# Kernel tuning notes

Measured on AMD Instinct MI355X. Metric: run time of the kernel, lower is better.

## Reference

```python
import jax, jax.numpy as jnp
import numpy as np

N_HEAD = 16
D_MODEL = 1024
D_HEAD = D_MODEL // N_HEAD  # 64
B, S = 1, 4096


def setup_inputs() -> dict:
    key = jax.random.key(0)
    ks = jax.random.split(key, 7)
    q = jax.random.normal(ks[0], (B, S, D_MODEL), dtype=jnp.float32)
    k = jax.random.normal(ks[1], (B, S, D_MODEL), dtype=jnp.float32)
    v = jax.random.normal(ks[2], (B, S, D_MODEL), dtype=jnp.float32)
    mask = jnp.ones((S, S), dtype=bool)
    # params match torch.rand init (uniform [0,1)); use uniform here too
    w_q = jax.random.uniform(ks[3], (D_MODEL, D_MODEL), dtype=jnp.float32)
    w_k = jax.random.uniform(ks[4], (D_HEAD, D_MODEL), dtype=jnp.float32)
    w_v = jax.random.uniform(ks[5], (D_HEAD, D_MODEL), dtype=jnp.float32)
    w_out = jax.random.uniform(ks[6], (D_MODEL, D_MODEL), dtype=jnp.float32)
    return {"q": q, "k": k, "v": v, "mask": mask,
            "w_q": w_q, "w_k": w_k, "w_v": w_v, "w_out": w_out}


def reference(q, k, v, mask, w_q, w_k, w_v, w_out):
    # F.linear(x, W) == x @ W.T
    query = q @ w_q.T                      # [b, n, d_model]
    key = k @ w_k.T                        # [b, s, d_head]  (single shared KV head)
    value = v @ w_v.T                      # [b, s, d_head]
    b, n, _ = query.shape
    query = query.reshape(b, n, N_HEAD, D_HEAD).transpose(0, 2, 1, 3)  # b h n d
    scores = jnp.einsum('bhnd,bsd->bhns', query, key) / jnp.sqrt(jnp.float32(D_HEAD))
    scores = jnp.where(mask[None, None], scores, jnp.float32(-jnp.inf))
    attn = jax.nn.softmax(scores, axis=-1)             # [b, h, n, s]
    out = jnp.einsum('bhns,bsd->bhnd', attn, value)    # [b, h, n, d]
    out = out.transpose(0, 2, 1, 3).reshape(b, n, D_MODEL)
    return out @ w_out.T
```

## Files before the change

kernel.cpp:

```cpp
#include <hip/hip_runtime.h>
#include <cstdint>
#include <cstddef>

#define S_LEN   4096
#define DM      1024
#define NHEAD   16
#define DH      64
#define SPLITS  4

typedef short bf16x8 __attribute__((ext_vector_type(8)));
typedef _Float16 f16x8 __attribute__((ext_vector_type(8)));
typedef float f32x4  __attribute__((ext_vector_type(4)));

__device__ __forceinline__ unsigned short f2bf(float x) {
    uint32_t u = __float_as_uint(x);
    u += 0x7fffu + ((u >> 16) & 1u);
    return (unsigned short)(u >> 16);
}
__device__ __forceinline__ float bf2f(unsigned short u) {
    return __uint_as_float(((uint32_t)u) << 16);
}
__device__ __forceinline__ unsigned pack_bf2(float a, float b) {
    return (unsigned)f2bf(a) | ((unsigned)f2bf(b) << 16);
}
__device__ __forceinline__ unsigned short f2h(float x) {
    _Float16 h = (_Float16)x;
    return __builtin_bit_cast(unsigned short, h);
}
__device__ __forceinline__ unsigned pack_h2(float a, float b) {
    return __builtin_bit_cast(unsigned, __builtin_amdgcn_cvt_pkrtz(a, b));
}
__device__ __forceinline__ void gl_lds16(const unsigned short* g, unsigned short* l) {
    __builtin_amdgcn_global_load_lds(
        (const __attribute__((address_space(1))) unsigned int*)g,
        (__attribute__((address_space(3))) unsigned int*)l, 16, 0, 0);
}
__device__ __forceinline__ void split8(const float4& a0, const float4& a1,
                                       ushort4& h0, ushort4& h1,
                                       ushort4& l0, ushort4& l1) {
    h0.x = f2bf(a0.x); l0.x = f2bf(a0.x - bf2f(h0.x));
    h0.y = f2bf(a0.y); l0.y = f2bf(a0.y - bf2f(h0.y));
    h0.z = f2bf(a0.z); l0.z = f2bf(a0.z - bf2f(h0.z));
    h0.w = f2bf(a0.w); l0.w = f2bf(a0.w - bf2f(h0.w));
    h1.x = f2bf(a1.x); l1.x = f2bf(a1.x - bf2f(h1.x));
    h1.y = f2bf(a1.y); l1.y = f2bf(a1.y - bf2f(h1.y));
    h1.z = f2bf(a1.z); l1.z = f2bf(a1.z - bf2f(h1.z));
    h1.w = f2bf(a1.w); l1.w = f2bf(a1.w - bf2f(h1.w));
}

__launch_bounds__(256)
__global__ void pre_kernel(const float* __restrict__ kin, const float* __restrict__ vin,
                           const float* __restrict__ wk, const float* __restrict__ wv,
                           const float* __restrict__ q, const float* __restrict__ wq,
                           const float* __restrict__ wo,
                           unsigned short* __restrict__ Kf, unsigned short* __restrict__ Vtf,
                           unsigned short* __restrict__ qh, unsigned short* __restrict__ ql,
                           unsigned short* __restrict__ wqh, unsigned short* __restrict__ wql,
                           unsigned short* __restrict__ woh)
{
    __shared__ unsigned short As_h[64][72];
    __shared__ unsigned short Bs_h[64][72];
    __shared__ unsigned short As_l[64][72];
    __shared__ unsigned short Bs_l[64][72];

    const int tid = threadIdx.x;
    const int bx  = blockIdx.x;

    if (bx >= 128) {
        const int G1 = 1048576, GW = 262144;
        int i = (bx - 128) * 256 + tid;
        const float* src; unsigned short* h; unsigned short* l = nullptr; int off;
        if (i < G1)            { src = q;  h = qh;  l = ql;  off = i; }
        else if (i < G1 + GW)  { src = wq; h = wqh; l = wql; off = i - G1; }
        else                   { src = wo; h = woh;          off = i - G1 - GW; }
        float4 vv = reinterpret_cast<const float4*>(src)[off];
        ushort4 hh;
        hh.x = f2bf(vv.x); hh.y = f2bf(vv.y); hh.z = f2bf(vv.z); hh.w = f2bf(vv.w);
        reinterpret_cast<ushort4*>(h)[off] = hh;
        if (l) {
            ushort4 ll;
            ll.x = f2bf(vv.x - bf2f(hh.x)); ll.y = f2bf(vv.y - bf2f(hh.y));
            ll.z = f2bf(vv.z - bf2f(hh.z)); ll.w = f2bf(vv.w - bf2f(hh.w));
            reinterpret_cast<ushort4*>(l)[off] = ll;
        }
        return;
    }

    const int wave = tid >> 6;
    const int lane = tid & 63;
    const int lm   = lane & 15;
    const int quad = lane >> 4;
    const bool isK = (bx < 64);
    const int m0   = (bx & 63) * 64;
    const float* A = isK ? kin : vin;
    const float* B = isK ? wk : wv;

    f32x4 acc[4] = {};

    for (int kc = 0; kc < DM; kc += 64) {
        __syncthreads();
#pragma unroll
        for (int i = 0; i < 2; ++i) {
            int c   = tid + i * 256;
            int r   = c >> 3;
            int col = (c & 7) * 8;
            float4 a0 = *(const float4*)&A[(size_t)(m0 + r) * DM + kc + col];
            float4 a1 = *(const float4*)&A[(size_t)(m0 + r) * DM + kc + col + 4];
            float4 b0 = *(const float4*)&B[(size_t)r * DM + kc + col];
            float4 b1 = *(const float4*)&B[(size_t)r * DM + kc + col + 4];
            ushort4 h0, h1, l0, l1;
            split8(a0, a1, h0, h1, l0, l1);
            *(ushort4*)&As_h[r][col] = h0;  *(ushort4*)&As_h[r][col + 4] = h1;
            if (isK) { *(ushort4*)&As_l[r][col] = l0;  *(ushort4*)&As_l[r][col + 4] = l1; }
            split8(b0, b1, h0, h1, l0, l1);
            *(ushort4*)&Bs_h[r][col] = h0;  *(ushort4*)&Bs_h[r][col + 4] = h1;
            if (isK) { *(ushort4*)&Bs_l[r][col] = l0;  *(ushort4*)&Bs_l[r][col + 4] = l1; }
        }
        __syncthreads();
#pragma unroll
        for (int kk = 0; kk < 64; kk += 32) {
            bf16x8 bh = *(const bf16x8*)&Bs_h[wave * 16 + lm][kk + quad * 8];
            bf16x8 bl;
            if (isK) bl = *(const bf16x8*)&Bs_l[wave * 16 + lm][kk + quad * 8];
#pragma unroll
            for (int ms = 0; ms < 4; ++ms) {
                bf16x8 ah = *(const bf16x8*)&As_h[ms * 16 + lm][kk + quad * 8];
                acc[ms] = __builtin_amdgcn_mfma_f32_16x16x32_bf16(ah, bh, acc[ms], 0, 0, 0);
                if (isK) {
                    bf16x8 al = *(const bf16x8*)&As_l[ms * 16 + lm][kk + quad * 8];
                    acc[ms] = __builtin_amdgcn_mfma_f32_16x16x32_bf16(ah, bl, acc[ms], 0, 0, 0);
                    acc[ms] = __builtin_amdgcn_mfma_f32_16x16x32_bf16(al, bh, acc[ms], 0, 0, 0);
                }
            }
        }
    }

#pragma unroll
    for (int ms = 0; ms < 4; ++ms)
#pragma unroll
        for (int r = 0; r < 4; ++r) {
            int row = m0 + ms * 16 + quad * 4 + r;
            int col = wave * 16 + lm;
            if (isK) Kf[(size_t)row * DH + col] = f2h(acc[ms][r]);
            else     Vtf[(size_t)col * S_LEN + row] = f2h(acc[ms][r]);
        }
}

__launch_bounds__(256)
__global__ void gemm_big(const unsigned short* __restrict__ Ah,
                         const unsigned short* __restrict__ Al,
                         const unsigned short* __restrict__ Bh,
                         const unsigned short* __restrict__ Bl,
                         unsigned short* __restrict__ Ch,
                         int M, int N, int K, int ldc)
{
    __shared__ unsigned short As_h[2][8192];
    __shared__ unsigned short Bs_h[2][8192];
    __shared__ unsigned short As_l[2][8192];
    __shared__ unsigned short Bs_l[2][8192];

    const int tid  = threadIdx.x;
    const int wave = tid >> 6;
    const int lane = tid & 63;
    const int lm   = lane & 15;
    const int quad = lane >> 4;
    const int wm   = wave >> 1;
    const int wn   = wave & 1;
    const int m0   = blockIdx.x * 128;
    const int n0   = blockIdx.y * 128;

    int srow[4], scol[4];
#pragma unroll
    for (int i = 0; i < 4; ++i) {
        int f = i * 256 + tid;
        srow[i] = f >> 3;
        scol[i] = ((f & 7) ^ (srow[i] & 7)) * 8;
    }

    auto stage = [&](int b, int kc) {
#pragma unroll
        for (int i = 0; i < 4; ++i) {
            const int dst = (i * 256 + wave * 64) * 8;
            gl_lds16(&Ah[(size_t)(m0 + srow[i]) * K + kc + scol[i]], &As_h[b][dst]);
            gl_lds16(&Bh[(size_t)(n0 + srow[i]) * K + kc + scol[i]], &Bs_h[b][dst]);
            gl_lds16(&Al[(size_t)(m0 + srow[i]) * K + kc + scol[i]], &As_l[b][dst]);
            gl_lds16(&Bl[(size_t)(n0 + srow[i]) * K + kc + scol[i]], &Bs_l[b][dst]);
        }
    };

    stage(0, 0);

    f32x4 acc[4][4] = {};
    const int nkc = K / 64;

    for (int it = 0; it < nkc; ++it) {
        const int b = it & 1;
        __syncthreads();
        if (it + 1 < nkc) stage(b ^ 1, (it + 1) * 64);

#pragma unroll
        for (int kk = 0; kk < 2; ++kk) {
            bf16x8 bh[4], bl[4];
#pragma unroll
            for (int ns = 0; ns < 4; ++ns) {
                const int off = (wn * 64 + ns * 16 + lm) * 64 + ((kk * 4 + quad) ^ (lm & 7)) * 8;
                bh[ns] = *(const bf16x8*)&Bs_h[b][off];
                bl[ns] = *(const bf16x8*)&Bs_l[b][off];
            }
#pragma unroll
            for (int ms = 0; ms < 4; ++ms) {
                const int off = (wm * 64 + ms * 16 + lm) * 64 + ((kk * 4 + quad) ^ (lm & 7)) * 8;
                bf16x8 ah = *(const bf16x8*)&As_h[b][off];
                bf16x8 al = *(const bf16x8*)&As_l[b][off];
#pragma unroll
                for (int ns = 0; ns < 4; ++ns) {
                    acc[ms][ns] = __builtin_amdgcn_mfma_f32_16x16x32_bf16(ah, bh[ns], acc[ms][ns], 0, 0, 0);
                    acc[ms][ns] = __builtin_amdgcn_mfma_f32_16x16x32_bf16(ah, bl[ns], acc[ms][ns], 0, 0, 0);
                    acc[ms][ns] = __builtin_amdgcn_mfma_f32_16x16x32_bf16(al, bh[ns], acc[ms][ns], 0, 0, 0);
                }
            }
        }
    }

#pragma unroll
    for (int ms = 0; ms < 4; ++ms)
#pragma unroll
        for (int ns = 0; ns < 4; ++ns)
#pragma unroll
            for (int r = 0; r < 4; ++r) {
                int row = m0 + wm * 64 + ms * 16 + quad * 4 + r;
                int col = n0 + wn * 64 + ns * 16 + lm;
                Ch[(size_t)row * ldc + col] = f2h(acc[ms][ns][r]);
            }
}

__launch_bounds__(256)
__global__ void flash_kernel(const unsigned short* __restrict__ Qf,
                             const unsigned short* __restrict__ Kf,
                             const unsigned short* __restrict__ Vt,
                             unsigned short* __restrict__ Op,
                             float* __restrict__ Mb,
                             float* __restrict__ Lb)
{
    __shared__ unsigned short Ks[2][4096];
    __shared__ unsigned short Vs[2][4096];

    const int tid  = threadIdx.x;
    const int wave = tid >> 6;
    const int lane = tid & 63;
    const int lm   = lane & 15;
    const int quad = lane >> 4;
    const int q0   = blockIdx.x * 128;
    const int h    = blockIdx.y;
    const int sp   = blockIdx.z;
    const int kbase = sp * (S_LEN / SPLITS);
    const int NIT  = S_LEN / SPLITS / 64;
    const float c  = 0.125f * 1.44269504f;

    const int r0 = tid >> 3,         c0 = ((tid & 7) ^ (r0 & 7)) * 8;
    const int r1 = (tid + 256) >> 3, c1 = ((tid & 7) ^ (r1 & 7)) * 8;
    const int ldsA = wave * 512;
    const int ldsB = 2048 + wave * 512;

    auto stage = [&](int kt, int b) {
        gl_lds16(&Kf[(size_t)(kt + r0) * DH + c0], &Ks[b][ldsA]);
        gl_lds16(&Kf[(size_t)(kt + r1) * DH + c1], &Ks[b][ldsB]);
        gl_lds16(&Vt[(size_t)r0 * S_LEN + kt + c0], &Vs[b][ldsA]);
        gl_lds16(&Vt[(size_t)r1 * S_LEN + kt + c1], &Vs[b][ldsB]);
    };

    stage(kbase, 0);

    f16x8 qf[2][2];
#pragma unroll
    for (int nb = 0; nb < 2; ++nb)
#pragma unroll
        for (int kk = 0; kk < 2; ++kk) {
            size_t idx = (size_t)(q0 + wave * 32 + nb * 16 + lm) * DM + h * DH + kk * 32 + quad * 8;
            qf[nb][kk] = *(const f16x8*)&Qf[idx];
        }

    f32x4 oacc[2][4] = {};
    float m_run[2] = {-1e30f, -1e30f}, l_run[2] = {0.f, 0.f};

    for (int it = 0; it < NIT; ++it) {
        const int b = it & 1;
        const int kt = kbase + it * 64;
        __syncthreads();
        if (it + 1 < NIT) stage(kt + 64, b ^ 1);

        f32x4 sacc[2][4] = {};
#pragma unroll
        for (int kk = 0; kk < 2; ++kk) {
#pragma unroll
            for (int ms = 0; ms < 4; ++ms) {
                const int off = (ms * 16 + lm) * 64 + ((4 * kk + quad) ^ (lm & 7)) * 8;
                f16x8 kfr = *(const f16x8*)&Ks[b][off];
#pragma unroll
                for (int nb = 0; nb < 2; ++nb)
                    sacc[nb][ms] = __builtin_amdgcn_mfma_f32_16x16x32_f16(kfr, qf[nb][kk], sacc[nb][ms], 0, 0, 0);
            }
        }

        float mn[2];
#pragma unroll
        for (int nb = 0; nb < 2; ++nb) {
            float mx = -1e30f;
#pragma unroll
            for (int ms = 0; ms < 4; ++ms)
#pragma unroll
                for (int r = 0; r < 4; ++r) mx = fmaxf(mx, sacc[nb][ms][r]);
            mx = fmaxf(mx, __shfl_xor(mx, 16));
            mx = fmaxf(mx, __shfl_xor(mx, 32));
            mn[nb] = fmaxf(m_run[nb], mx);
        }

        if (__any((mn[0] > m_run[0]) || (mn[1] > m_run[1]))) {
#pragma unroll
            for (int mq = 0; mq < 2; ++mq) {
                float alpha = __builtin_amdgcn_exp2f((m_run[mq] - mn[mq]) * c);
                l_run[mq] *= alpha;
                m_run[mq] = mn[mq];
                float ar[4];
#pragma unroll
                for (int r = 0; r < 4; ++r) ar[r] = __shfl(alpha, quad * 4 + r);
#pragma unroll
                for (int nd = 0; nd < 4; ++nd)
#pragma unroll
                    for (int r = 0; r < 4; ++r) oacc[mq][nd][r] *= ar[r];
            }
        }

        unsigned pk[2][4][2];
#pragma unroll
        for (int nb = 0; nb < 2; ++nb) {
            float mc = m_run[nb] * c;
            float ps = 0.f;
#pragma unroll
            for (int ms = 0; ms < 4; ++ms) {
                float pr[4];
#pragma unroll
                for (int r = 0; r < 4; ++r) {
                    pr[r] = __builtin_amdgcn_exp2f(fmaf(sacc[nb][ms][r], c, -mc));
                    ps += pr[r];
                }
                pk[nb][ms][0] = pack_h2(pr[0], pr[1]);
                pk[nb][ms][1] = pack_h2(pr[2], pr[3]);
            }
            ps += __shfl_xor(ps, 16);
            ps += __shfl_xor(ps, 32);
            l_run[nb] += ps;
        }

#pragma unroll
        for (int kb = 0; kb < 2; ++kb) {
            f16x8 pa[2];
#pragma unroll
            for (int nb = 0; nb < 2; ++nb) {
                unsigned af[4] __attribute__((aligned(16)));
#pragma unroll
                for (int d = 0; d < 4; ++d) {
                    int srcl = ((2 * quad + (d >> 1)) & 3) * 16 + lm;
                    unsigned v_lo = (unsigned)__shfl((int)pk[nb][2 * kb][d & 1], srcl);
                    unsigned v_hi = (unsigned)__shfl((int)pk[nb][2 * kb + 1][d & 1], srcl);
                    af[d] = (quad < 2) ? v_lo : v_hi;
                }
                pa[nb] = *(f16x8*)af;
            }
#pragma unroll
            for (int nd = 0; nd < 4; ++nd) {
                const int off = (nd * 16 + lm) * 64 + ((4 * kb + quad) ^ (lm & 7)) * 8;
                f16x8 vb = *(const f16x8*)&Vs[b][off];
#pragma unroll
                for (int nb = 0; nb < 2; ++nb)
                    oacc[nb][nd] = __builtin_amdgcn_mfma_f32_16x16x32_f16(pa[nb], vb, oacc[nb][nd], 0, 0, 0);
            }
        }
    }

    unsigned short* Osp = Op + (size_t)sp * NHEAD * S_LEN * DH;
#pragma unroll
    for (int mq = 0; mq < 2; ++mq) {
#pragma unroll
        for (int nd = 0; nd < 4; ++nd)
#pragma unroll
            for (int r = 0; r < 4; ++r) {
                int q = q0 + wave * 32 + mq * 16 + quad * 4 + r;
                Osp[((size_t)h * S_LEN + q) * DH + nd * 16 + lm] = f2bf(oacc[mq][nd][r]);
            }
        if (quad == 0) {
            int q = q0 + wave * 32 + mq * 16 + lm;
            Mb[(size_t)sp * NHEAD * S_LEN + h * S_LEN + q] = m_run[mq];
            Lb[(size_t)sp * NHEAD * S_LEN + h * S_LEN + q] = l_run[mq];
        }
    }
}

__launch_bounds__(256)
__global__ void out_proj(const unsigned short* __restrict__ Op,
                         const float* __restrict__ Mb,
                         const float* __restrict__ Lb,
                         const unsigned short* __restrict__ Wo,
                         float* __restrict__ out)
{
    __shared__ unsigned short As[64][72];
    __shared__ unsigned short Bs[128][72];

    const int tid  = threadIdx.x;
    const int wave = tid >> 6;
    const int lane = tid & 63;
    const int lm   = lane & 15;
    const int quad = lane >> 4;
    const int m0   = blockIdx.x * 64;
    const int n0   = blockIdx.y * 128;
    const float c  = 0.125f * 1.44269504f;
    const int HS   = NHEAD * S_LEN;
    const size_t OSP = (size_t)NHEAD * S_LEN * DH;

    f32x4 acc[4][2] = {};

    for (int it = 0; it < 16; ++it) {
        __syncthreads();
#pragma unroll
        for (int i = 0; i < 2; ++i) {
            int cc  = tid + i * 256;
            int r   = cc >> 3;
            int col = (cc & 7) * 8;
            int q   = m0 + r;
            int hq  = it * S_LEN + q;
            float m_i[SPLITS], l_i[SPLITS];
            float mm = -1e30f;
#pragma unroll
            for (int s = 0; s < SPLITS; ++s) {
                m_i[s] = Mb[s * HS + hq];
                l_i[s] = Lb[s * HS + hq];
                mm = fmaxf(mm, m_i[s]);
            }
            float w_i[SPLITS], denom = 0.f;
#pragma unroll
            for (int s = 0; s < SPLITS; ++s) {
                w_i[s] = __builtin_amdgcn_exp2f((m_i[s] - mm) * c);
                denom += l_i[s] * w_i[s];
            }
            float inv = 1.0f / denom;
#pragma unroll
            for (int s = 0; s < SPLITS; ++s) w_i[s] *= inv;

            size_t base = ((size_t)it * S_LEN + q) * DH + col;
            uint4 u[SPLITS];
#pragma unroll
            for (int s = 0; s < SPLITS; ++s) u[s] = *(const uint4*)&Op[s * OSP + base];
            unsigned mrg[4];
#pragma unroll
            for (int d = 0; d < 4; ++d) {
                float a = 0.f, b = 0.f;
#pragma unroll
                for (int s = 0; s < SPLITS; ++s) {
                    unsigned uu = ((const unsigned*)&u[s])[d];
                    a = fmaf(bf2f((unsigned short)(uu & 0xffff)), w_i[s], a);
                    b = fmaf(bf2f((unsigned short)(uu >> 16)),    w_i[s], b);
                }
                mrg[d] = pack_bf2(a, b);
            }
            *(uint4*)&As[r][col] = *(uint4*)mrg;
        }
#pragma unroll
        for (int i = 0; i < 4; ++i) {
            int cc  = tid + i * 256;
            int r   = cc >> 3;
            int col = (cc & 7) * 8;
            *(uint4*)&Bs[r][col] = *(const uint4*)&Wo[(size_t)(n0 + r) * DM + it * 64 + col];
        }
        __syncthreads();
#pragma unroll
        for (int kk = 0; kk < 64; kk += 32) {
            bf16x8 bh[2];
#pragma unroll
            for (int ns = 0; ns < 2; ++ns)
                bh[ns] = *(const bf16x8*)&Bs[wave * 32 + ns * 16 + lm][kk + quad * 8];
#pragma unroll
            for (int ms = 0; ms < 4; ++ms) {
                bf16x8 ah = *(const bf16x8*)&As[ms * 16 + lm][kk + quad * 8];
#pragma unroll
                for (int ns = 0; ns < 2; ++ns)
                    acc[ms][ns] = __builtin_amdgcn_mfma_f32_16x16x32_bf16(ah, bh[ns], acc[ms][ns], 0, 0, 0);
            }
        }
    }

#pragma unroll
    for (int ms = 0; ms < 4; ++ms)
#pragma unroll
        for (int ns = 0; ns < 2; ++ns)
#pragma unroll
            for (int r = 0; r < 4; ++r) {
                int row = m0 + ms * 16 + quad * 4 + r;
                int col = n0 + wave * 32 + ns * 16 + lm;
                out[(size_t)row * DM + col] = acc[ms][ns][r];
            }
}

extern "C" void kernel_launch(void* const* d_in, const int* in_sizes, int n_in,
                              void* d_out, int out_size, void* d_ws, size_t ws_size,
                              hipStream_t stream)
{
    (void)in_sizes; (void)n_in; (void)out_size; (void)ws_size;
    const float* q     = (const float*)d_in[0];
    const float* k     = (const float*)d_in[1];
    const float* v     = (const float*)d_in[2];
    const float* w_q   = (const float*)d_in[4];
    const float* w_k   = (const float*)d_in[5];
    const float* w_v   = (const float*)d_in[6];
    const float* w_out = (const float*)d_in[7];
    float* out = (float*)d_out;

    char* ws = (char*)d_ws;
    size_t off = 0;
    auto alloc = [&](size_t bytes) -> unsigned short* {
        unsigned short* p = (unsigned short*)(ws + off);
        off += (bytes + 255) & ~(size_t)255;
        return p;
    };
    const size_t SZ_QKV = (size_t)S_LEN * DM * 2;
    const size_t SZ_WQ  = (size_t)DM * DM * 2;
    const size_t SZ_KV  = (size_t)S_LEN * DH * 2;

    unsigned short* qh  = alloc(SZ_QKV);
    unsigned short* ql  = alloc(SZ_QKV);
    unsigned short* wqh = alloc(SZ_WQ);
    unsigned short* wql = alloc(SZ_WQ);
    unsigned short* woh = alloc(SZ_WQ);
    unsigned short* Qf  = alloc(SZ_QKV);
    unsigned short* Kf  = alloc(SZ_KV);
    unsigned short* Vtf = alloc(SZ_KV);
    unsigned short* Op  = alloc(SPLITS * NHEAD * SZ_KV);
    float* Mb = (float*)alloc(SPLITS * NHEAD * S_LEN * 4);
    float* Lb = (float*)alloc(SPLITS * NHEAD * S_LEN * 4);

    pre_kernel<<<dim3(6272), 256, 0, stream>>>(k, v, w_k, w_v, q, w_q, w_out,
                                               Kf, Vtf, qh, ql, wqh, wql, woh);

    gemm_big<<<dim3(32, 8), 256, 0, stream>>>(qh, ql, wqh, wql, Qf, S_LEN, DM, DM, DM);

    flash_kernel<<<dim3(32, 16, SPLITS), 256, 0, stream>>>(Qf, Kf, Vtf, Op, Mb, Lb);

    out_proj<<<dim3(64, 8), 256, 0, stream>>>(Op, Mb, Lb, woh, out);
}
```

Before: 397.7 us.

## Double KV tile to 128 keys per iteration and halve split-K count

```diff
diff --git a/kernel.cpp b/kernel.cpp
--- a/kernel.cpp
+++ b/kernel.cpp
@@ -6,7 +6,7 @@
 #define DM      1024
 #define NHEAD   16
 #define DH      64
-#define SPLITS  4
+#define SPLITS  2
 
 typedef short bf16x8 __attribute__((ext_vector_type(8)));
 typedef _Float16 f16x8 __attribute__((ext_vector_type(8)));
@@ -242,8 +242,8 @@
                              float* __restrict__ Mb,
                              float* __restrict__ Lb)
 {
-    __shared__ unsigned short Ks[2][4096];
-    __shared__ unsigned short Vs[2][4096];
+    __shared__ unsigned short Ks[2][8192];
+    __shared__ unsigned short Vs[2][8192];
 
     const int tid  = threadIdx.x;
     const int wave = tid >> 6;
@@ -254,19 +254,24 @@
     const int h    = blockIdx.y;
     const int sp   = blockIdx.z;
     const int kbase = sp * (S_LEN / SPLITS);
-    const int NIT  = S_LEN / SPLITS / 64;
+    const int NIT  = S_LEN / SPLITS / 128;
     const float c  = 0.125f * 1.44269504f;
 
-    const int r0 = tid >> 3,         c0 = ((tid & 7) ^ (r0 & 7)) * 8;
-    const int r1 = (tid + 256) >> 3, c1 = ((tid & 7) ^ (r1 & 7)) * 8;
-    const int ldsA = wave * 512;
-    const int ldsB = 2048 + wave * 512;
+    int kr[4], kcol[4], vr[4], vcol[4];
+#pragma unroll
+    for (int i = 0; i < 4; ++i) {
+        int f = i * 256 + tid;
+        kr[i] = f >> 3;  kcol[i] = ((f & 7) ^ (kr[i] & 7)) * 8;
+        vr[i] = f >> 4;  vcol[i] = ((f & 15) ^ (vr[i] & 15)) * 8;
+    }
 
     auto stage = [&](int kt, int b) {
-        gl_lds16(&Kf[(size_t)(kt + r0) * DH + c0], &Ks[b][ldsA]);
-        gl_lds16(&Kf[(size_t)(kt + r1) * DH + c1], &Ks[b][ldsB]);
-        gl_lds16(&Vt[(size_t)r0 * S_LEN + kt + c0], &Vs[b][ldsA]);
-        gl_lds16(&Vt[(size_t)r1 * S_LEN + kt + c1], &Vs[b][ldsB]);
+#pragma unroll
+        for (int i = 0; i < 4; ++i) {
+            const int dst = (i * 256 + wave * 64) * 8;
+            gl_lds16(&Kf[(size_t)(kt + kr[i]) * DH + kcol[i]], &Ks[b][dst]);
+            gl_lds16(&Vt[(size_t)vr[i] * S_LEN + kt + vcol[i]], &Vs[b][dst]);
+        }
     };
 
     stage(kbase, 0);
@@ -285,31 +290,34 @@
 
     for (int it = 0; it < NIT; ++it) {
         const int b = it & 1;
-        const int kt = kbase + it * 64;
+        const int kt = kbase + it * 128;
         __syncthreads();
-        if (it + 1 < NIT) stage(kt + 64, b ^ 1);
-
-        f32x4 sacc[2][4] = {};
-#pragma unroll
-        for (int kk = 0; kk < 2; ++kk) {
-#pragma unroll
-            for (int ms = 0; ms < 4; ++ms) {
-                const int off = (ms * 16 + lm) * 64 + ((4 * kk + quad) ^ (lm & 7)) * 8;
-                f16x8 kfr = *(const f16x8*)&Ks[b][off];
-#pragma unroll
-                for (int nb = 0; nb < 2; ++nb)
-                    sacc[nb][ms] = __builtin_amdgcn_mfma_f32_16x16x32_f16(kfr, qf[nb][kk], sacc[nb][ms], 0, 0, 0);
-            }
-        }
+        if (it + 1 < NIT) stage(kt + 128, b ^ 1);
+
+        f32x4 sacc[2][2][4] = {};
+#pragma unroll
+        for (int t = 0; t < 2; ++t)
+#pragma unroll
+            for (int kk = 0; kk < 2; ++kk)
+#pragma unroll
+                for (int ms = 0; ms < 4; ++ms) {
+                    const int off = (t * 64 + ms * 16 + lm) * 64 + ((4 * kk + quad) ^ (lm & 7)) * 8;
+                    f16x8 kfr = *(const f16x8*)&Ks[b][off];
+#pragma unroll
+                    for (int nb = 0; nb < 2; ++nb)
+                        sacc[nb][t][ms] = __builtin_amdgcn_mfma_f32_16x16x32_f16(kfr, qf[nb][kk], sacc[nb][t][ms], 0, 0, 0);
+                }
 
         float mn[2];
 #pragma unroll
         for (int nb = 0; nb < 2; ++nb) {
             float mx = -1e30f;
 #pragma unroll
-            for (int ms = 0; ms < 4; ++ms)
-#pragma unroll
-                for (int r = 0; r < 4; ++r) mx = fmaxf(mx, sacc[nb][ms][r]);
+            for (int t = 0; t < 2; ++t)
+#pragma unroll
+                for (int ms = 0; ms < 4; ++ms)
+#pragma unroll
+                    for (int r = 0; r < 4; ++r) mx = fmaxf(mx, sacc[nb][t][ms][r]);
             mx = fmaxf(mx, __shfl_xor(mx, 16));
             mx = fmaxf(mx, __shfl_xor(mx, 32));
             mn[nb] = fmaxf(m_run[nb], mx);
@@ -331,51 +339,56 @@
             }
         }
 
-        unsigned pk[2][4][2];
+        unsigned pk[2][2][4][2];
 #pragma unroll
         for (int nb = 0; nb < 2; ++nb) {
             float mc = m_run[nb] * c;
             float ps = 0.f;
 #pragma unroll
-            for (int ms = 0; ms < 4; ++ms) {
-                float pr[4];
-#pragma unroll
-                for (int r = 0; r < 4; ++r) {
-                    pr[r] = __builtin_amdgcn_exp2f(fmaf(sacc[nb][ms][r], c, -mc));
-                    ps += pr[r];
-                }
-                pk[nb][ms][0] = pack_h2(pr[0], pr[1]);
-                pk[nb][ms][1] = pack_h2(pr[2], pr[3]);
-            }
+            for (int t = 0; t < 2; ++t)
+#pragma unroll
+                for (int ms = 0; ms < 4; ++ms) {
+                    float pr[4];
+#pragma unroll
+                    for (int r = 0; r < 4; ++r) {
+                        pr[r] = __builtin_amdgcn_exp2f(fmaf(sacc[nb][t][ms][r], c, -mc));
+                        ps += pr[r];
+                    }
+                    pk[nb][t][ms][0] = pack_h2(pr[0], pr[1]);
+                    pk[nb][t][ms][1] = pack_h2(pr[2], pr[3]);
+                }
             ps += __shfl_xor(ps, 16);
             ps += __shfl_xor(ps, 32);
             l_run[nb] += ps;
         }
 
 #pragma unroll
-        for (int kb = 0; kb < 2; ++kb) {
-            f16x8 pa[2];
-#pragma unroll
-            for (int nb = 0; nb < 2; ++nb) {
-                unsigned af[4] __attribute__((aligned(16)));
-#pragma unroll
-                for (int d = 0; d < 4; ++d) {
-                    int srcl = ((2 * quad + (d >> 1)) & 3) * 16 + lm;
-                    unsigned v_lo = (unsigned)__shfl((int)pk[nb][2 * kb][d & 1], srcl);
-                    unsigned v_hi = (unsigned)__shfl((int)pk[nb][2 * kb + 1][d & 1], srcl);
-                    af[d] = (quad < 2) ? v_lo : v_hi;
-                }
-                pa[nb] = *(f16x8*)af;
-            }
-#pragma unroll
-            for (int nd = 0; nd < 4; ++nd) {
-                const int off = (nd * 16 + lm) * 64 + ((4 * kb + quad) ^ (lm & 7)) * 8;
-                f16x8 vb = *(const f16x8*)&Vs[b][off];
-#pragma unroll
-                for (int nb = 0; nb < 2; ++nb)
-                    oacc[nb][nd] = __builtin_amdgcn_mfma_f32_16x16x32_f16(pa[nb], vb, oacc[nb][nd], 0, 0, 0);
-            }
-        }
+        for (int t = 0; t < 2; ++t)
+#pragma unroll
+            for (int kb = 0; kb < 2; ++kb) {
+                f16x8 pa[2];
+#pragma unroll
+                for (int nb = 0; nb < 2; ++nb) {
+                    unsigned af[4] __attribute__((aligned(16)));
+#pragma unroll
+                    for (int d = 0; d < 4; ++d) {
+                        int srcl = ((2 * quad + (d >> 1)) & 3) * 16 + lm;
+                        unsigned v_lo = (unsigned)__shfl((int)pk[nb][t][2 * kb][d & 1], srcl);
+                        unsigned v_hi = (unsigned)__shfl((int)pk[nb][t][2 * kb + 1][d & 1], srcl);
+                        af[d] = (quad < 2) ? v_lo : v_hi;
+                    }
+                    pa[nb] = *(f16x8*)af;
+                }
+                const int kbg = t * 2 + kb;
+#pragma unroll
+                for (int nd = 0; nd < 4; ++nd) {
+                    const int off = (nd * 16 + lm) * 128 + (((kbg * 4 + quad) ^ lm) * 8);
+                    f16x8 vb = *(const f16x8*)&Vs[b][off];
+#pragma unroll
+                    for (int nb = 0; nb < 2; ++nb)
+                        oacc[nb][nd] = __builtin_amdgcn_mfma_f32_16x16x32_f16(pa[nb], vb, oacc[nb][nd], 0, 0, 0);
+                }
+            }
     }
 
     unsigned short* Osp = Op + (size_t)sp * NHEAD * S_LEN * DH;
```

After: 374.7 us. -5.8%, faster.
